# Optimization experiments

Measured on AMD Instinct MI355X. Metric: run time of the kernel, lower is better.

## Reference

```python
import jax, jax.numpy as jnp
import numpy as np

E = 8                 # n_experts
CAPACITY_FACTOR = 1.25

B, T, H, I = 4, 1024, 2048, 1408


def setup_inputs() -> dict:
    key = jax.random.key(0)
    k0, k1, k2, k3, k4 = jax.random.split(key, 5)
    x = jax.random.normal(k0, (B, T, H), jnp.float32)
    Wr = jax.random.normal(k1, (E, H), jnp.float32) * 0.02   # router proj (no bias)
    Wg = jax.random.normal(k2, (E, I, H), jnp.float32) * 0.02  # gate_proj per expert
    Wu = jax.random.normal(k3, (E, I, H), jnp.float32) * 0.02  # up_proj per expert
    Wd = jax.random.normal(k4, (E, H, I), jnp.float32) * 0.02  # down_proj per expert
    return {"x": x, "Wr": Wr, "Wg": Wg, "Wu": Wu, "Wd": Wd}


def reference(x, Wr, Wg, Wu, Wd):
    Bb, Tt, Hh = x.shape
    N = Bb * Tt
    cap = max(1, int(CAPACITY_FACTOR * (N * 2 / E)))
    xf = x.reshape(N, Hh)

    # --- Top2Router (noise_std=0 -> no noise) ---
    logits = jnp.einsum('nh,eh->ne', xf, Wr)          # [N, E]
    gate = jax.nn.softmax(logits, axis=-1)
    top2_val, top2_idx = jax.lax.top_k(gate, 2)        # [N, 2]

    # --- capacity masking, matching torch loop order: slot k=0 over all
    # tokens (flat order), then slot k=1; within an expert the first `cap`
    # assignments are kept ---
    flat_idx = jnp.concatenate([top2_idx[:, 0], top2_idx[:, 1]])   # [2N]
    flat_val = jnp.concatenate([top2_val[:, 0], top2_val[:, 1]])   # [2N]
    onehot = jax.nn.one_hot(flat_idx, E, dtype=jnp.int32)          # [2N, E]
    rank = (jnp.cumsum(onehot, axis=0) * onehot).sum(-1)           # inclusive rank within expert
    keep = rank <= cap                                             # [2N]
    w_assign = jnp.where(keep, flat_val, 0.0)

    # combine weights per (token, expert); top-2 experts per token are distinct
    tok = jnp.tile(jnp.arange(N), 2)
    comb = jnp.zeros((N, E), x.dtype).at[tok, flat_idx].add(w_assign)  # [N, E]

    # --- per-expert SwiGLU FFN applied densely, combined with gate weights ---
    g = jax.nn.silu(jnp.einsum('nh,eih->eni', xf, Wg))  # [E, N, I]
    u = jnp.einsum('nh,eih->eni', xf, Wu)               # [E, N, I]
    out_e = jnp.einsum('eni,ehi->enh', g * u, Wd)       # [E, N, H]
    y = jnp.einsum('ne,enh->nh', comb, out_e)           # [N, H]
    return y.reshape(Bb, Tt, Hh)
```

## Files before the change

### kernel.cpp

```cpp
#include <hip/hip_runtime.h>
#include <hip/hip_bf16.h>

#define N_TOK 4096
#define H_DIM 2048
#define I_DIM 1408
#define E_NUM 8
#define CAP   1280

typedef __hip_bfloat16 bf16;
typedef __bf16 bf16x8 __attribute__((ext_vector_type(8)));
typedef float f32x4 __attribute__((ext_vector_type(4)));

__device__ inline void gld_lds16(const void* g, void* l) {
    __builtin_amdgcn_global_load_lds((const __attribute__((address_space(1))) void*)g,
                                     (__attribute__((address_space(3))) void*)l,
                                     16, 0, 0);
}

__global__ void cvt4(const float* __restrict__ s, unsigned short* __restrict__ d, long n) {
    long i = ((long)blockIdx.x * blockDim.x + threadIdx.x) * 4;
    if (i >= n) return;
    float4 v = *(const float4*)(s + i);
    union { unsigned short u[4]; ushort2 h[2]; } o;
    bf16 b0 = __float2bfloat16(v.x);
    bf16 b1 = __float2bfloat16(v.y);
    bf16 b2 = __float2bfloat16(v.z);
    bf16 b3 = __float2bfloat16(v.w);
    o.u[0] = *(unsigned short*)&b0;
    o.u[1] = *(unsigned short*)&b1;
    o.u[2] = *(unsigned short*)&b2;
    o.u[3] = *(unsigned short*)&b3;
    *(ushort2*)(d + i)     = o.h[0];
    *(ushort2*)(d + i + 2) = o.h[1];
}

__global__ void router_k(const float* __restrict__ x, const float* __restrict__ Wr,
                         float* __restrict__ top_val, int* __restrict__ top_idx) {
    int tok  = (blockIdx.x * blockDim.x + threadIdx.x) >> 6;
    int lane = threadIdx.x & 63;
    if (tok >= N_TOK) return;
    const float* xr = x + (size_t)tok * H_DIM;
    float acc[E_NUM];
#pragma unroll
    for (int e = 0; e < E_NUM; e++) acc[e] = 0.f;
    for (int h = lane; h < H_DIM; h += 64) {
        float xv = xr[h];
#pragma unroll
        for (int e = 0; e < E_NUM; e++) acc[e] += xv * Wr[e * H_DIM + h];
    }
#pragma unroll
    for (int e = 0; e < E_NUM; e++) {
#pragma unroll
        for (int off = 32; off > 0; off >>= 1) acc[e] += __shfl_xor(acc[e], off, 64);
    }
    if (lane == 0) {
        float mx = acc[0];
#pragma unroll
        for (int e = 1; e < E_NUM; e++) mx = fmaxf(mx, acc[e]);
        float p[E_NUM], s = 0.f;
#pragma unroll
        for (int e = 0; e < E_NUM; e++) { p[e] = __expf(acc[e] - mx); s += p[e]; }
        float inv = 1.f / s;
#pragma unroll
        for (int e = 0; e < E_NUM; e++) p[e] *= inv;
        int i0 = 0;
#pragma unroll
        for (int e = 1; e < E_NUM; e++) if (p[e] > p[i0]) i0 = e;
        int i1 = -1;
#pragma unroll
        for (int e = 0; e < E_NUM; e++) {
            if (e == i0) continue;
            if (i1 < 0 || p[e] > p[i1]) i1 = e;
        }
        top_idx[tok * 2]     = i0;
        top_idx[tok * 2 + 1] = i1;
        top_val[tok * 2]     = p[i0];
        top_val[tok * 2 + 1] = p[i1];
    }
}

__global__ void assign_k(const int* __restrict__ top_idx, const float* __restrict__ top_val,
                         int* __restrict__ toklist, float* __restrict__ wlist,
                         int* __restrict__ counts) {
    const int T = 256;
    const int CH = (2 * N_TOK) / T;
    int t = threadIdx.x;
    for (int i = t; i < E_NUM * CAP; i += T) { toklist[i] = N_TOK; wlist[i] = 0.f; }
    __shared__ int cnt[T][E_NUM];
    int local[E_NUM];
#pragma unroll
    for (int e = 0; e < E_NUM; e++) local[e] = 0;
    for (int q = 0; q < CH; q++) {
        int j = t * CH + q;
        int slot = j >> 12;
        int tok  = j & 4095;
        int e = top_idx[tok * 2 + slot];
        local[e]++;
    }
#pragma unroll
    for (int e = 0; e < E_NUM; e++) cnt[t][e] = local[e];
    __syncthreads();
    if (t < E_NUM) {
        int run = 0;
        for (int i = 0; i < T; i++) { int c = cnt[i][t]; cnt[i][t] = run; run += c; }
        counts[t] = run < CAP ? run : CAP;
    }
    __syncthreads();
    int run[E_NUM];
#pragma unroll
    for (int e = 0; e < E_NUM; e++) run[e] = cnt[t][e];
    for (int q = 0; q < CH; q++) {
        int j = t * CH + q;
        int slot = j >> 12;
        int tok  = j & 4095;
        int e = top_idx[tok * 2 + slot];
        int rank = ++run[e];
        if (rank <= CAP) {
            toklist[e * CAP + rank - 1] = tok;
            wlist[e * CAP + rank - 1]   = top_val[tok * 2 + slot];
        }
    }
}

template <int MODE>
__global__ __launch_bounds__(256)
void expert_gemm(const unsigned short* __restrict__ A, const unsigned short* __restrict__ W,
                 unsigned short* __restrict__ gbuf, unsigned short* __restrict__ hbuf,
                 float* __restrict__ out,
                 const int* __restrict__ toklist, const float* __restrict__ wlist,
                 const int* __restrict__ counts, int Ndim, int K) {
    const int e  = blockIdx.z;
    const int m0 = blockIdx.y * 128;
    const int n0 = blockIdx.x * 128;
    if (m0 >= counts[e]) return;

    __shared__ unsigned short As[128 * 32];
    __shared__ unsigned short Bs[128 * 32];

    const int t  = threadIdx.x;
    const int r0 = t >> 2;
    const int c8 = (t & 3) * 8;

    const unsigned short *aP0, *aP1;
    if (MODE < 2) {
        int tok0 = toklist[e * CAP + m0 + r0];
        int tok1 = toklist[e * CAP + m0 + r0 + 64];
        aP0 = A + (size_t)tok0 * K + c8;
        aP1 = A + (size_t)tok1 * K + c8;
    } else {
        aP0 = A + ((size_t)e * CAP + m0 + r0) * (size_t)K + c8;
        aP1 = aP0 + (size_t)64 * K;
    }
    const unsigned short* bP0 = W + (size_t)e * Ndim * K + (size_t)(n0 + r0) * K + c8;
    const unsigned short* bP1 = bP0 + (size_t)64 * K;

    unsigned short* ldsA0 = As + t * 8;
    unsigned short* ldsA1 = ldsA0 + 64 * 32;
    unsigned short* ldsB0 = Bs + t * 8;
    unsigned short* ldsB1 = ldsB0 + 64 * 32;

    const int lane = t & 63;
    const int wave = t >> 6;
    const int wm   = (wave & 1) * 64;
    const int wn   = (wave >> 1) * 64;
    const int l15  = lane & 15;
    const int quad = lane >> 4;

    f32x4 acc[4][4];
#pragma unroll
    for (int i = 0; i < 4; i++)
#pragma unroll
        for (int j = 0; j < 4; j++) acc[i][j] = (f32x4){0.f, 0.f, 0.f, 0.f};

    for (int k = 0; k < K; k += 32) {
        gld_lds16(aP0, ldsA0);
        gld_lds16(aP1, ldsA1);
        gld_lds16(bP0, ldsB0);
        gld_lds16(bP1, ldsB1);
        aP0 += 32; aP1 += 32; bP0 += 32; bP1 += 32;
        __syncthreads();
        bf16x8 af[4], bfr[4];
#pragma unroll
        for (int i = 0; i < 4; i++)
            af[i] = *(const bf16x8*)(As + (wm + i * 16 + l15) * 32 + quad * 8);
#pragma unroll
        for (int j = 0; j < 4; j++)
            bfr[j] = *(const bf16x8*)(Bs + (wn + j * 16 + l15) * 32 + quad * 8);
#pragma unroll
        for (int i = 0; i < 4; i++)
#pragma unroll
            for (int j = 0; j < 4; j++)
                acc[i][j] = __builtin_amdgcn_mfma_f32_16x16x32_bf16(af[i], bfr[j], acc[i][j], 0, 0, 0);
        __syncthreads();
    }

    if (MODE == 0) {
#pragma unroll
        for (int i = 0; i < 4; i++) {
            int mb = m0 + wm + i * 16 + quad * 4;
#pragma unroll
            for (int r = 0; r < 4; r++) {
                size_t rowoff = ((size_t)e * CAP + mb + r) * I_DIM;
#pragma unroll
                for (int j = 0; j < 4; j++) {
                    int n = n0 + wn + j * 16 + l15;
                    float v = acc[i][j][r];
                    float sg = v / (1.f + __expf(-v));
                    bf16 b = __float2bfloat16(sg);
                    gbuf[rowoff + n] = *(unsigned short*)&b;
                }
            }
        }
    } else if (MODE == 1) {
#pragma unroll
        for (int i = 0; i < 4; i++) {
            int mb = m0 + wm + i * 16 + quad * 4;
#pragma unroll
            for (int r = 0; r < 4; r++) {
                size_t rowoff = ((size_t)e * CAP + mb + r) * I_DIM;
#pragma unroll
                for (int j = 0; j < 4; j++) {
                    int n = n0 + wn + j * 16 + l15;
                    unsigned short gu = gbuf[rowoff + n];
                    float sg = __bfloat162float(*(bf16*)&gu);
                    bf16 b = __float2bfloat16(sg * acc[i][j][r]);
                    hbuf[rowoff + n] = *(unsigned short*)&b;
                }
            }
        }
    } else {
#pragma unroll
        for (int i = 0; i < 4; i++) {
            int mb = m0 + wm + i * 16 + quad * 4;
#pragma unroll
            for (int r = 0; r < 4; r++) {
                int tok = toklist[e * CAP + mb + r];
                if (tok < N_TOK) {
                    float wgt = wlist[e * CAP + mb + r];
                    float* orow = out + (size_t)tok * H_DIM + n0 + wn + l15;
#pragma unroll
                    for (int j = 0; j < 4; j++)
                        atomicAdd(orow + j * 16, wgt * acc[i][j][r]);
                }
            }
        }
    }
}

extern "C" void kernel_launch(void* const* d_in, const int* in_sizes, int n_in,
                              void* d_out, int out_size, void* d_ws, size_t ws_size,
                              hipStream_t stream) {
    const float* x  = (const float*)d_in[0];
    const float* Wr = (const float*)d_in[1];
    const float* Wg = (const float*)d_in[2];
    const float* Wu = (const float*)d_in[3];
    const float* Wd = (const float*)d_in[4];
    float* out = (float*)d_out;

    char* p = (char*)d_ws;
    auto alloc = [&](size_t bytes) { char* r = p; p += (bytes + 255) & ~(size_t)255; return r; };
    unsigned short* xb   = (unsigned short*)alloc((size_t)(N_TOK + 1) * H_DIM * 2);
    unsigned short* Wgb  = (unsigned short*)alloc((size_t)E_NUM * I_DIM * H_DIM * 2);
    unsigned short* Wub  = (unsigned short*)alloc((size_t)E_NUM * I_DIM * H_DIM * 2);
    unsigned short* Wdb  = (unsigned short*)alloc((size_t)E_NUM * H_DIM * I_DIM * 2);
    unsigned short* gbuf = (unsigned short*)alloc((size_t)E_NUM * CAP * I_DIM * 2);
    unsigned short* hbuf = (unsigned short*)alloc((size_t)E_NUM * CAP * I_DIM * 2);
    float* top_val = (float*)alloc((size_t)N_TOK * 2 * 4);
    int*   top_idx = (int*)alloc((size_t)N_TOK * 2 * 4);
    int*   toklist = (int*)alloc((size_t)E_NUM * CAP * 4);
    float* wlist   = (float*)alloc((size_t)E_NUM * CAP * 4);
    int*   counts  = (int*)alloc((size_t)E_NUM * 4);

    hipMemsetAsync(out, 0, (size_t)N_TOK * H_DIM * 4, stream);
    hipMemsetAsync(xb + (size_t)N_TOK * H_DIM, 0, H_DIM * 2, stream);

    long nx = (long)N_TOK * H_DIM;
    long nw = (long)E_NUM * I_DIM * H_DIM;
    cvt4<<<dim3((unsigned)((nx / 4 + 255) / 256)), dim3(256), 0, stream>>>(x, xb, nx);
    cvt4<<<dim3((unsigned)((nw / 4 + 255) / 256)), dim3(256), 0, stream>>>(Wg, Wgb, nw);
    cvt4<<<dim3((unsigned)((nw / 4 + 255) / 256)), dim3(256), 0, stream>>>(Wu, Wub, nw);
    cvt4<<<dim3((unsigned)((nw / 4 + 255) / 256)), dim3(256), 0, stream>>>(Wd, Wdb, nw);

    router_k<<<dim3(N_TOK / 4), dim3(256), 0, stream>>>(x, Wr, top_val, top_idx);
    assign_k<<<dim3(1), dim3(256), 0, stream>>>(top_idx, top_val, toklist, wlist, counts);

    dim3 g1(I_DIM / 128, CAP / 128, E_NUM);
    expert_gemm<0><<<g1, dim3(256), 0, stream>>>(xb, Wgb, gbuf, nullptr, nullptr, toklist, wlist, counts, I_DIM, H_DIM);
    expert_gemm<1><<<g1, dim3(256), 0, stream>>>(xb, Wub, gbuf, hbuf, nullptr, toklist, wlist, counts, I_DIM, H_DIM);
    dim3 g2(H_DIM / 128, CAP / 128, E_NUM);
    expert_gemm<2><<<g2, dim3(256), 0, stream>>>(hbuf, Wdb, nullptr, nullptr, out, toklist, wlist, counts, H_DIM, I_DIM);
}
```

Baseline: 727.9 us.

## Fuse gate and up projections into one GEMM and batch weight conversions

Gate and up projections are merged into a single kernel that loads each gathered token tile once and accumulates both outputs, then applies SiLU(g)*u directly when writing hbuf. This drops the gbuf intermediate write and read, and halves the gathered activation loads. The three weight-conversion launches are folded into one 3D-grid launch. The fused kernel doubles accumulator registers (128 floats per thread), which may lower occupancy or cause spills.

Measured after the change: 759.9 us. 1.04x slower.

```diff
diff --git a/kernel.cpp b/kernel.cpp
--- a/kernel.cpp
+++ b/kernel.cpp
@@ -8,6 +8,7 @@
 #define CAP   1280
 
 typedef __hip_bfloat16 bf16;
+typedef unsigned short us;
 typedef __bf16 bf16x8 __attribute__((ext_vector_type(8)));
 typedef float f32x4 __attribute__((ext_vector_type(4)));
 
@@ -17,21 +18,31 @@
                                      16, 0, 0);
 }
 
-__global__ void cvt4(const float* __restrict__ s, unsigned short* __restrict__ d, long n) {
-    long i = ((long)blockIdx.x * blockDim.x + threadIdx.x) * 4;
+__device__ inline void cvt_body(const float* __restrict__ s, us* __restrict__ d, long i, long n) {
     if (i >= n) return;
     float4 v = *(const float4*)(s + i);
-    union { unsigned short u[4]; ushort2 h[2]; } o;
+    union { us u[4]; ushort2 h[2]; } o;
     bf16 b0 = __float2bfloat16(v.x);
     bf16 b1 = __float2bfloat16(v.y);
     bf16 b2 = __float2bfloat16(v.z);
     bf16 b3 = __float2bfloat16(v.w);
-    o.u[0] = *(unsigned short*)&b0;
-    o.u[1] = *(unsigned short*)&b1;
-    o.u[2] = *(unsigned short*)&b2;
-    o.u[3] = *(unsigned short*)&b3;
+    o.u[0] = *(us*)&b0; o.u[1] = *(us*)&b1; o.u[2] = *(us*)&b2; o.u[3] = *(us*)&b3;
     *(ushort2*)(d + i)     = o.h[0];
     *(ushort2*)(d + i + 2) = o.h[1];
+}
+
+__global__ void cvt4(const float* __restrict__ s, us* __restrict__ d, long n) {
+    long i = ((long)blockIdx.x * blockDim.x + threadIdx.x) * 4;
+    cvt_body(s, d, i, n);
+}
+
+__global__ void cvt_w3(const float* __restrict__ s0, const float* __restrict__ s1,
+                       const float* __restrict__ s2, us* __restrict__ d0,
+                       us* __restrict__ d1, us* __restrict__ d2, long n) {
+    long i = ((long)blockIdx.x * blockDim.x + threadIdx.x) * 4;
+    const float* s = blockIdx.z == 0 ? s0 : (blockIdx.z == 1 ? s1 : s2);
+    us* d = blockIdx.z == 0 ? d0 : (blockIdx.z == 1 ? d1 : d2);
+    cvt_body(s, d, i, n);
 }
 
 __global__ void router_k(const float* __restrict__ x, const float* __restrict__ Wr,
@@ -122,42 +133,35 @@
     }
 }
 
-template <int MODE>
 __global__ __launch_bounds__(256)
-void expert_gemm(const unsigned short* __restrict__ A, const unsigned short* __restrict__ W,
-                 unsigned short* __restrict__ gbuf, unsigned short* __restrict__ hbuf,
-                 float* __restrict__ out,
-                 const int* __restrict__ toklist, const float* __restrict__ wlist,
-                 const int* __restrict__ counts, int Ndim, int K) {
+void gateup_gemm(const us* __restrict__ A, const us* __restrict__ Wg,
+                 const us* __restrict__ Wu, us* __restrict__ hbuf,
+                 const int* __restrict__ toklist, const int* __restrict__ counts) {
     const int e  = blockIdx.z;
     const int m0 = blockIdx.y * 128;
     const int n0 = blockIdx.x * 128;
     if (m0 >= counts[e]) return;
 
-    __shared__ unsigned short As[128 * 32];
-    __shared__ unsigned short Bs[128 * 32];
+    __shared__ us As[128 * 32];
+    __shared__ us Gs[128 * 32];
+    __shared__ us Us[128 * 32];
 
     const int t  = threadIdx.x;
     const int r0 = t >> 2;
     const int c8 = (t & 3) * 8;
 
-    const unsigned short *aP0, *aP1;
-    if (MODE < 2) {
-        int tok0 = toklist[e * CAP + m0 + r0];
-        int tok1 = toklist[e * CAP + m0 + r0 + 64];
-        aP0 = A + (size_t)tok0 * K + c8;
-        aP1 = A + (size_t)tok1 * K + c8;
-    } else {
-        aP0 = A + ((size_t)e * CAP + m0 + r0) * (size_t)K + c8;
-        aP1 = aP0 + (size_t)64 * K;
-    }
-    const unsigned short* bP0 = W + (size_t)e * Ndim * K + (size_t)(n0 + r0) * K + c8;
-    const unsigned short* bP1 = bP0 + (size_t)64 * K;
-
-    unsigned short* ldsA0 = As + t * 8;
-    unsigned short* ldsA1 = ldsA0 + 64 * 32;
-    unsigned short* ldsB0 = Bs + t * 8;
-    unsigned short* ldsB1 = ldsB0 + 64 * 32;
+    int tok0 = toklist[e * CAP + m0 + r0];
+    int tok1 = toklist[e * CAP + m0 + r0 + 64];
+    const us* aP0 = A + (size_t)tok0 * H_DIM + c8;
+    const us* aP1 = A + (size_t)tok1 * H_DIM + c8;
+    const us* gP0 = Wg + ((size_t)e * I_DIM + n0 + r0) * H_DIM + c8;
+    const us* gP1 = gP0 + (size_t)64 * H_DIM;
+    const us* uP0 = Wu + ((size_t)e * I_DIM + n0 + r0) * H_DIM + c8;
+    const us* uP1 = uP0 + (size_t)64 * H_DIM;
+
+    us* lA0 = As + t * 8; us* lA1 = lA0 + 64 * 32;
+    us* lG0 = Gs + t * 8; us* lG1 = lG0 + 64 * 32;
+    us* lU0 = Us + t * 8; us* lU1 = lU0 + 64 * 32;
 
     const int lane = t & 63;
     const int wave = t >> 6;
@@ -166,17 +170,105 @@
     const int l15  = lane & 15;
     const int quad = lane >> 4;
 
+    f32x4 ag[4][4], au[4][4];
+#pragma unroll
+    for (int i = 0; i < 4; i++)
+#pragma unroll
+        for (int j = 0; j < 4; j++) {
+            ag[i][j] = (f32x4){0.f, 0.f, 0.f, 0.f};
+            au[i][j] = (f32x4){0.f, 0.f, 0.f, 0.f};
+        }
+
+    for (int k = 0; k < H_DIM; k += 32) {
+        gld_lds16(aP0, lA0);
+        gld_lds16(aP1, lA1);
+        gld_lds16(gP0, lG0);
+        gld_lds16(gP1, lG1);
+        gld_lds16(uP0, lU0);
+        gld_lds16(uP1, lU1);
+        aP0 += 32; aP1 += 32; gP0 += 32; gP1 += 32; uP0 += 32; uP1 += 32;
+        __syncthreads();
+        bf16x8 af[4], bg[4], bu[4];
+#pragma unroll
+        for (int i = 0; i < 4; i++)
+            af[i] = *(const bf16x8*)(As + (wm + i * 16 + l15) * 32 + quad * 8);
+#pragma unroll
+        for (int j = 0; j < 4; j++) {
+            bg[j] = *(const bf16x8*)(Gs + (wn + j * 16 + l15) * 32 + quad * 8);
+            bu[j] = *(const bf16x8*)(Us + (wn + j * 16 + l15) * 32 + quad * 8);
+        }
+#pragma unroll
+        for (int i = 0; i < 4; i++)
+#pragma unroll
+            for (int j = 0; j < 4; j++) {
+                ag[i][j] = __builtin_amdgcn_mfma_f32_16x16x32_bf16(af[i], bg[j], ag[i][j], 0, 0, 0);
+                au[i][j] = __builtin_amdgcn_mfma_f32_16x16x32_bf16(af[i], bu[j], au[i][j], 0, 0, 0);
+            }
+        __syncthreads();
+    }
+
+#pragma unroll
+    for (int i = 0; i < 4; i++) {
+        int mb = m0 + wm + i * 16 + quad * 4;
+#pragma unroll
+        for (int r = 0; r < 4; r++) {
+            size_t rowoff = ((size_t)e * CAP + mb + r) * I_DIM;
+#pragma unroll
+            for (int j = 0; j < 4; j++) {
+                int n = n0 + wn + j * 16 + l15;
+                float g = ag[i][j][r];
+                float u = au[i][j][r];
+                float h = (g / (1.f + __expf(-g))) * u;
+                bf16 b = __float2bfloat16(h);
+                hbuf[rowoff + n] = *(us*)&b;
+            }
+        }
+    }
+}
+
+__global__ __launch_bounds__(256)
+void down_gemm(const us* __restrict__ A, const us* __restrict__ W,
+               float* __restrict__ out,
+               const int* __restrict__ toklist, const float* __restrict__ wlist,
+               const int* __restrict__ counts) {
+    const int e  = blockIdx.z;
+    const int m0 = blockIdx.y * 128;
+    const int n0 = blockIdx.x * 128;
+    if (m0 >= counts[e]) return;
+
+    __shared__ us As[128 * 32];
+    __shared__ us Bs[128 * 32];
+
+    const int t  = threadIdx.x;
+    const int r0 = t >> 2;
+    const int c8 = (t & 3) * 8;
+
+    const us* aP0 = A + ((size_t)e * CAP + m0 + r0) * (size_t)I_DIM + c8;
+    const us* aP1 = aP0 + (size_t)64 * I_DIM;
+    const us* bP0 = W + ((size_t)e * H_DIM + n0 + r0) * (size_t)I_DIM + c8;
+    const us* bP1 = bP0 + (size_t)64 * I_DIM;
+
+    us* lA0 = As + t * 8; us* lA1 = lA0 + 64 * 32;
+    us* lB0 = Bs + t * 8; us* lB1 = lB0 + 64 * 32;
+
+    const int lane = t & 63;
+    const int wave = t >> 6;
+    const int wm   = (wave & 1) * 64;
+    const int wn   = (wave >> 1) * 64;
+    const int l15  = lane & 15;
+    const int quad = lane >> 4;
+
     f32x4 acc[4][4];
 #pragma unroll
     for (int i = 0; i < 4; i++)
 #pragma unroll
         for (int j = 0; j < 4; j++) acc[i][j] = (f32x4){0.f, 0.f, 0.f, 0.f};
 
-    for (int k = 0; k < K; k += 32) {
-        gld_lds16(aP0, ldsA0);
-        gld_lds16(aP1, ldsA1);
-        gld_lds16(bP0, ldsB0);
-        gld_lds16(bP1, ldsB1);
+    for (int k = 0; k < I_DIM; k += 32) {
+        gld_lds16(aP0, lA0);
+        gld_lds16(aP1, lA1);
+        gld_lds16(bP0, lB0);
+        gld_lds16(bP1, lB1);
         aP0 += 32; aP1 += 32; bP0 += 32; bP1 += 32;
         __syncthreads();
         bf16x8 af[4], bfr[4];
@@ -194,54 +286,18 @@
         __syncthreads();
     }
 
-    if (MODE == 0) {
-#pragma unroll
-        for (int i = 0; i < 4; i++) {
-            int mb = m0 + wm + i * 16 + quad * 4;
-#pragma unroll
-            for (int r = 0; r < 4; r++) {
-                size_t rowoff = ((size_t)e * CAP + mb + r) * I_DIM;
-#pragma unroll
-                for (int j = 0; j < 4; j++) {
-                    int n = n0 + wn + j * 16 + l15;
-                    float v = acc[i][j][r];
-                    float sg = v / (1.f + __expf(-v));
-                    bf16 b = __float2bfloat16(sg);
-                    gbuf[rowoff + n] = *(unsigned short*)&b;
-                }
-            }
-        }
-    } else if (MODE == 1) {
-#pragma unroll
-        for (int i = 0; i < 4; i++) {
-            int mb = m0 + wm + i * 16 + quad * 4;
-#pragma unroll
-            for (int r = 0; r < 4; r++) {
-                size_t rowoff = ((size_t)e * CAP + mb + r) * I_DIM;
-#pragma unroll
-                for (int j = 0; j < 4; j++) {
-                    int n = n0 + wn + j * 16 + l15;
-                    unsigned short gu = gbuf[rowoff + n];
-                    float sg = __bfloat162float(*(bf16*)&gu);
-                    bf16 b = __float2bfloat16(sg * acc[i][j][r]);
-                    hbuf[rowoff + n] = *(unsigned short*)&b;
-                }
-            }
-        }
-    } else {
-#pragma unroll
-        for (int i = 0; i < 4; i++) {
-            int mb = m0 + wm + i * 16 + quad * 4;
-#pragma unroll
-            for (int r = 0; r < 4; r++) {
-                int tok = toklist[e * CAP + mb + r];
-                if (tok < N_TOK) {
-                    float wgt = wlist[e * CAP + mb + r];
-                    float* orow = out + (size_t)tok * H_DIM + n0 + wn + l15;
-#pragma unroll
-                    for (int j = 0; j < 4; j++)
-                        atomicAdd(orow + j * 16, wgt * acc[i][j][r]);
-                }
+#pragma unroll
+    for (int i = 0; i < 4; i++) {
+        int mb = m0 + wm + i * 16 + quad * 4;
+#pragma unroll
+        for (int r = 0; r < 4; r++) {
+            int tok = toklist[e * CAP + mb + r];
+            if (tok < N_TOK) {
+                float wgt = wlist[e * CAP + mb + r];
+                float* orow = out + (size_t)tok * H_DIM + n0 + wn + l15;
+#pragma unroll
+                for (int j = 0; j < 4; j++)
+                    atomicAdd(orow + j * 16, wgt * acc[i][j][r]);
             }
         }
     }
@@ -259,12 +315,11 @@
 
     char* p = (char*)d_ws;
     auto alloc = [&](size_t bytes) { char* r = p; p += (bytes + 255) & ~(size_t)255; return r; };
-    unsigned short* xb   = (unsigned short*)alloc((size_t)(N_TOK + 1) * H_DIM * 2);
-    unsigned short* Wgb  = (unsigned short*)alloc((size_t)E_NUM * I_DIM * H_DIM * 2);
-    unsigned short* Wub  = (unsigned short*)alloc((size_t)E_NUM * I_DIM * H_DIM * 2);
-    unsigned short* Wdb  = (unsigned short*)alloc((size_t)E_NUM * H_DIM * I_DIM * 2);
-    unsigned short* gbuf = (unsigned short*)alloc((size_t)E_NUM * CAP * I_DIM * 2);
-    unsigned short* hbuf = (unsigned short*)alloc((size_t)E_NUM * CAP * I_DIM * 2);
+    us* xb   = (us*)alloc((size_t)(N_TOK + 1) * H_DIM * 2);
+    us* Wgb  = (us*)alloc((size_t)E_NUM * I_DIM * H_DIM * 2);
+    us* Wub  = (us*)alloc((size_t)E_NUM * I_DIM * H_DIM * 2);
+    us* Wdb  = (us*)alloc((size_t)E_NUM * H_DIM * I_DIM * 2);
+    us* hbuf = (us*)alloc((size_t)E_NUM * CAP * I_DIM * 2);
     float* top_val = (float*)alloc((size_t)N_TOK * 2 * 4);
     int*   top_idx = (int*)alloc((size_t)N_TOK * 2 * 4);
     int*   toklist = (int*)alloc((size_t)E_NUM * CAP * 4);
@@ -277,16 +332,14 @@
     long nx = (long)N_TOK * H_DIM;
     long nw = (long)E_NUM * I_DIM * H_DIM;
     cvt4<<<dim3((unsigned)((nx / 4 + 255) / 256)), dim3(256), 0, stream>>>(x, xb, nx);
-    cvt4<<<dim3((unsigned)((nw / 4 + 255) / 256)), dim3(256), 0, stream>>>(Wg, Wgb, nw);
-    cvt4<<<dim3((unsigned)((nw / 4 + 255) / 256)), dim3(256), 0, stream>>>(Wu, Wub, nw);
-    cvt4<<<dim3((unsigned)((nw / 4 + 255) / 256)), dim3(256), 0, stream>>>(Wd, Wdb, nw);
+    cvt_w3<<<dim3((unsigned)((nw / 4 + 255) / 256), 1, 3), dim3(256), 0, stream>>>(
+        Wg, Wu, Wd, Wgb, Wub, Wdb, nw);
 
     router_k<<<dim3(N_TOK / 4), dim3(256), 0, stream>>>(x, Wr, top_val, top_idx);
     assign_k<<<dim3(1), dim3(256), 0, stream>>>(top_idx, top_val, toklist, wlist, counts);
 
     dim3 g1(I_DIM / 128, CAP / 128, E_NUM);
-    expert_gemm<0><<<g1, dim3(256), 0, stream>>>(xb, Wgb, gbuf, nullptr, nullptr, toklist, wlist, counts, I_DIM, H_DIM);
-    expert_gemm<1><<<g1, dim3(256), 0, stream>>>(xb, Wub, gbuf, hbuf, nullptr, toklist, wlist, counts, I_DIM, H_DIM);
+    gateup_gemm<<<g1, dim3(256), 0, stream>>>(xb, Wgb, Wub, hbuf, toklist, counts);
     dim3 g2(H_DIM / 128, CAP / 128, E_NUM);
-    expert_gemm<2><<<g2, dim3(256), 0, stream>>>(hbuf, Wdb, nullptr, nullptr, out, toklist, wlist, counts, H_DIM, I_DIM);
-}
+    down_gemm<<<g2, dim3(256), 0, stream>>>(hbuf, Wdb, out, toklist, wlist, counts);
+}
```
